# Kernel optimization log

Measured on AMD Instinct MI355X. Metric: run time of the kernel, lower is better.

## Reference

```python
import jax, jax.numpy as jnp
import numpy as np

DIM = 1024
HEAD_DIM = 64
NUM_HEADS = DIM // HEAD_DIM
SCALE = HEAD_DIM ** -0.5


def setup_inputs() -> dict:
    key = jax.random.key(0)
    ks = jax.random.split(key, 12)
    b, n = 4, 2048
    std = DIM ** -0.5
    inp = {
        'words': jax.random.normal(ks[0], (b, n, DIM), jnp.float32),
        'position': jax.random.normal(ks[1], (b, n, DIM), jnp.float32),
        'conscious': jax.random.normal(ks[2], (b, n, DIM), jnp.float32),
        # projection weights stored as [in, out] (torch Linear W^T)
        'w_wq': jax.random.normal(ks[3], (DIM, DIM), jnp.float32) * std,
        'w_wk': jax.random.normal(ks[4], (DIM, DIM), jnp.float32) * std,
        'w_wv': jax.random.normal(ks[5], (DIM, DIM), jnp.float32) * std,
        'w_pq': jax.random.normal(ks[6], (DIM, DIM), jnp.float32) * std,
        'w_pk': jax.random.normal(ks[7], (DIM, DIM), jnp.float32) * std,
        'w_cq': jax.random.normal(ks[8], (DIM, DIM), jnp.float32) * std,
        'w_ck': jax.random.normal(ks[9], (DIM, DIM), jnp.float32) * std,
        'w_out': jax.random.normal(ks[10], (DIM, DIM), jnp.float32) * std,
        'b_out': jax.random.normal(ks[11], (DIM,), jnp.float32) * 0.01,
    }
    return inp


def _heads(x):
    b, n, _ = x.shape
    return x.reshape(b, n, NUM_HEADS, HEAD_DIM).transpose(0, 2, 1, 3)  # b h n d


def reference(words, position, conscious, w_wq, w_wk, w_wv, w_pq, w_pk, w_cq, w_ck, w_out, b_out):
    # fused multi-source q/k: sum of three projections per source
    q = _heads(words @ w_wq + position @ w_pq + conscious @ w_cq)
    k = _heads(words @ w_wk + position @ w_pk + conscious @ w_ck)
    v = _heads(words @ w_wv)
    sim = jnp.einsum('bhid,bhjd->bhij', q, k) * SCALE
    attn = jax.nn.softmax(sim, axis=-1)
    out = jnp.einsum('bhij,bhjd->bhid', attn, v)
    b, h, n, d = out.shape
    out = out.transpose(0, 2, 1, 3).reshape(b, n, h * d)
    return out @ w_out + b_out
```

## Files before the change

### kernel.cpp

```cpp
#include <hip/hip_runtime.h>
#include <hip/hip_bf16.h>

typedef __bf16 bf16_t;
typedef __attribute__((ext_vector_type(8))) __bf16 bf16x8;
typedef __attribute__((ext_vector_type(4))) float f32x4;
typedef __attribute__((ext_vector_type(16))) float f32x16;

__device__ __forceinline__ void gld_lds16(const void* g, void* l) {
  __builtin_amdgcn_global_load_lds((const __attribute__((address_space(1))) void*)g,
                                   (__attribute__((address_space(3))) void*)l, 16, 0, 0);
}

__global__ __launch_bounds__(256) void cast_concat(
    const float* __restrict__ w, const float* __restrict__ p,
    const float* __restrict__ c, bf16_t* __restrict__ X)
{
  unsigned idx = blockIdx.x * 256u + threadIdx.x;
  unsigned src = idx >> 21;
  unsigned rem = idx & ((1u << 21) - 1);
  unsigned row = rem >> 8;
  unsigned k4  = (rem & 255u) * 4u;
  const float* s = (src == 0) ? w : (src == 1) ? p : c;
  f32x4 v = *(const f32x4*)(s + (size_t)row * 1024 + k4);
  ushort4 u;
  u.x = __builtin_bit_cast(unsigned short, (bf16_t)v[0]);
  u.y = __builtin_bit_cast(unsigned short, (bf16_t)v[1]);
  u.z = __builtin_bit_cast(unsigned short, (bf16_t)v[2]);
  u.w = __builtin_bit_cast(unsigned short, (bf16_t)v[3]);
  *(ushort4*)(X + (size_t)row * 3072 + src * 1024 + k4) = u;
}

__global__ __launch_bounds__(256) void transpose_all(
    const float* __restrict__ w_wq, const float* __restrict__ w_pq,
    const float* __restrict__ w_cq, const float* __restrict__ w_wk,
    const float* __restrict__ w_pk, const float* __restrict__ w_ck,
    const float* __restrict__ w_wv, const float* __restrict__ w_out,
    bf16_t* __restrict__ Wqkt, bf16_t* __restrict__ Wvt, bf16_t* __restrict__ Wot)
{
  __shared__ float t[32][33];
  const int z = blockIdx.z;
  const float* src; bf16_t* dst; int dstride, koff, roff;
  switch (z) {
    case 0: src = w_wq;  dst = Wqkt; dstride = 3072; koff = 0;    roff = 0;    break;
    case 1: src = w_pq;  dst = Wqkt; dstride = 3072; koff = 1024; roff = 0;    break;
    case 2: src = w_cq;  dst = Wqkt; dstride = 3072; koff = 2048; roff = 0;    break;
    case 3: src = w_wk;  dst = Wqkt; dstride = 3072; koff = 0;    roff = 1024; break;
    case 4: src = w_pk;  dst = Wqkt; dstride = 3072; koff = 1024; roff = 1024; break;
    case 5: src = w_ck;  dst = Wqkt; dstride = 3072; koff = 2048; roff = 1024; break;
    case 6: src = w_wv;  dst = Wvt;  dstride = 1024; koff = 0;    roff = 0;    break;
    default: src = w_out; dst = Wot; dstride = 1024; koff = 0;    roff = 0;    break;
  }
  int bx = blockIdx.x, by = blockIdx.y;
  int x = bx * 32 + threadIdx.x;
  int y0 = by * 32;
  for (int i = threadIdx.y; i < 32; i += 8)
    t[i][threadIdx.x] = src[(size_t)(y0 + i) * 1024 + x];
  __syncthreads();
  int n0 = bx * 32;
  for (int i = threadIdx.y; i < 32; i += 8)
    dst[(size_t)(n0 + i + roff) * dstride + koff + y0 + threadIdx.x] =
        (bf16_t)t[threadIdx.x][i];
}

__global__ __launch_bounds__(512, 2) void gemm256_qk(
    const bf16_t* __restrict__ A, int lda,
    const bf16_t* __restrict__ Bt, int K,
    bf16_t* __restrict__ Qo, bf16_t* __restrict__ Ko, float scale, int nbx)
{
  __shared__ bf16_t As[2][256 * 64];
  __shared__ bf16_t Bs[2][256 * 64];

  const int tid = threadIdx.x;
  const int wave = tid >> 6, lane = tid & 63;
  const int wm = wave >> 2, wn = wave & 3;
  const int lrow = lane & 15, lch = lane >> 4;

  const int nwg = gridDim.x, cpx = nwg >> 3;
  const int id  = blockIdx.x;
  const int swz = (id & 7) * cpx + (id >> 3);
  const int mb = swz / nbx, nb = swz % nbx;
  const int m0 = mb * 256, n0 = nb * 256;

  const int srow = tid >> 3, spp = tid & 7;

  auto STAGE = [&](int buf, int k0) {
#pragma unroll
    for (int i = 0; i < 4; ++i) {
      int r = i * 64 + srow;
      int gsw = (spp ^ (r & 7)) * 8;
      gld_lds16(A + (size_t)(m0 + r) * lda + k0 + gsw, &As[buf][r * 64 + spp * 8]);
    }
#pragma unroll
    for (int i = 0; i < 4; ++i) {
      int r = i * 64 + srow;
      int gsw = (spp ^ (r & 7)) * 8;
      gld_lds16(Bt + (size_t)(n0 + r) * K + k0 + gsw, &Bs[buf][r * 64 + spp * 8]);
    }
  };

  const int NT = K >> 6;
  STAGE(0, 0);
  STAGE(1, 64);

  f32x4 acc[8][4] = {};

  for (int kt = 0; kt < NT; ++kt) {
    const int cur = kt & 1;
    if (kt < NT - 1) {
      asm volatile("s_waitcnt vmcnt(8)" ::: "memory");
    } else {
      asm volatile("s_waitcnt vmcnt(0)" ::: "memory");
    }
    asm volatile("s_barrier" ::: "memory");

#pragma unroll
    for (int ks = 0; ks < 2; ++ks) {
      bf16x8 af[8], bfr[4];
#pragma unroll
      for (int m = 0; m < 8; ++m) {
        int r = wm * 128 + m * 16 + lrow;
        af[m] = *(const bf16x8*)&As[cur][r * 64 + (((ks * 4 + lch) ^ (r & 7)) * 8)];
      }
#pragma unroll
      for (int n = 0; n < 4; ++n) {
        int r = wn * 64 + n * 16 + lrow;
        bfr[n] = *(const bf16x8*)&Bs[cur][r * 64 + (((ks * 4 + lch) ^ (r & 7)) * 8)];
      }
      __builtin_amdgcn_s_setprio(1);
#pragma unroll
      for (int m = 0; m < 8; ++m)
#pragma unroll
        for (int n = 0; n < 4; ++n)
          acc[m][n] = __builtin_amdgcn_mfma_f32_16x16x32_bf16(af[m], bfr[n], acc[m][n], 0, 0, 0);
      __builtin_amdgcn_s_setprio(0);
    }

    asm volatile("s_waitcnt lgkmcnt(0)" ::: "memory");
    asm volatile("s_barrier" ::: "memory");
    if (kt + 2 < NT) STAGE(cur, (kt + 2) * 64);
  }

  const int g = lane >> 4, cl = lane & 15;
#pragma unroll
  for (int m = 0; m < 8; ++m) {
    int m_base = m0 + wm * 128 + m * 16 + g * 4;
    int bb = m_base >> 11, nn = m_base & 2047;
#pragma unroll
    for (int n = 0; n < 4; ++n) {
      int col = n0 + wn * 64 + n * 16 + cl;
      bf16_t* dst = (col < 1024) ? Qo : Ko;
      int cc2 = col & 1023;
      float sc = (col < 1024) ? scale : 1.0f;
      int h = cc2 >> 6, d = cc2 & 63;
      size_t base = ((size_t)(bb * 16 + h) * 2048 + nn) * 64 + d;
#pragma unroll
      for (int r = 0; r < 4; ++r)
        dst[base + (size_t)r * 64] = (bf16_t)(acc[m][n][r] * sc);
    }
  }
}

template<int EPI>
__global__ __launch_bounds__(256, 2) void gemm_bt(
    const bf16_t* __restrict__ A, int lda,
    const bf16_t* __restrict__ Bt, int K,
    void* __restrict__ Cout, const float* __restrict__ bias, float scale)
{
  __shared__ bf16_t As[128 * 32];
  __shared__ bf16_t Bs[128 * 32];
  const int tid  = threadIdx.x;
  const int wave = tid >> 6, lane = tid & 63;
  const int m0 = blockIdx.y * 128, n0 = blockIdx.x * 128;
  const int wr = (wave >> 1) * 64, wc = (wave & 1) * 64;
  const int lrow = lane & 15, lch = lane >> 4;

  f32x4 acc[4][4] = {};

  for (int k0 = 0; k0 < K; k0 += 32) {
    __syncthreads();
#pragma unroll
    for (int t = 0; t < 2; ++t) {
      int cc = t * 256 + tid;
      int row = cc >> 2, pp = cc & 3;
      int kswz = (pp ^ (row & 3)) * 8;
      gld_lds16(A  + (size_t)(m0 + row) * lda + k0 + kswz, &As[cc * 8]);
      gld_lds16(Bt + (size_t)(n0 + row) * K   + k0 + kswz, &Bs[cc * 8]);
    }
    __syncthreads();
    bf16x8 a[4], b[4];
#pragma unroll
    for (int i = 0; i < 4; ++i) {
      int r = wr + i * 16 + lrow;
      a[i] = *(const bf16x8*)&As[r * 32 + ((lch ^ (r & 3)) * 8)];
    }
#pragma unroll
    for (int i = 0; i < 4; ++i) {
      int r = wc + i * 16 + lrow;
      b[i] = *(const bf16x8*)&Bs[r * 32 + ((lch ^ (r & 3)) * 8)];
    }
#pragma unroll
    for (int i = 0; i < 4; ++i)
#pragma unroll
      for (int j = 0; j < 4; ++j)
        acc[i][j] = __builtin_amdgcn_mfma_f32_16x16x32_bf16(a[i], b[j], acc[i][j], 0, 0, 0);
  }

  const int g = lane >> 4, cl = lane & 15;
  if (EPI == 1) {
    bf16_t* Vo = (bf16_t*)Cout;
#pragma unroll
    for (int i = 0; i < 4; ++i) {
      int m_base = m0 + wr + i * 16 + g * 4;
      int bb = m_base >> 11, nn = m_base & 2047;
#pragma unroll
      for (int j = 0; j < 4; ++j) {
        int col = n0 + wc + j * 16 + cl;
        int h = col >> 6, d = col & 63;
        ushort4 u;
        u.x = __builtin_bit_cast(unsigned short, (bf16_t)acc[i][j][0]);
        u.y = __builtin_bit_cast(unsigned short, (bf16_t)acc[i][j][1]);
        u.z = __builtin_bit_cast(unsigned short, (bf16_t)acc[i][j][2]);
        u.w = __builtin_bit_cast(unsigned short, (bf16_t)acc[i][j][3]);
        *(ushort4*)(Vo + ((size_t)(bb * 16 + h) * 64 + d) * 2048 + nn) = u;
      }
    }
  } else {
    float* Co = (float*)Cout;
#pragma unroll
    for (int i = 0; i < 4; ++i) {
      int m_base = m0 + wr + i * 16 + g * 4;
#pragma unroll
      for (int j = 0; j < 4; ++j) {
        int col = n0 + wc + j * 16 + cl;
        float bv = bias[col];
#pragma unroll
        for (int r = 0; r < 4; ++r)
          Co[(size_t)(m_base + r) * 1024 + col] = acc[i][j][r] + bv;
      }
    }
  }
}

__global__ __launch_bounds__(512, 2) void attn_kernel(
    const bf16_t* __restrict__ Q, const bf16_t* __restrict__ Kb,
    const bf16_t* __restrict__ Vt, bf16_t* __restrict__ O)
{
  __shared__ bf16_t Ks[2][64 * 64];
  __shared__ bf16_t Vs[2][64 * 64];

  const int fid = blockIdx.x;
  const int swz = (fid & 7) * 64 + (fid >> 3);
  const int bh = swz >> 3, qt = swz & 7;
  const int bb = bh >> 4, h = bh & 15;

  const int tid = threadIdx.x, wave = tid >> 6, lane = tid & 63;
  const int lq = lane & 31;
  const int lh = lane >> 5;

  const bf16_t* Qb    = Q  + ((size_t)bh * 2048 + qt * 256) * 64;
  const bf16_t* Kbase = Kb + (size_t)bh * 2048 * 64;
  const bf16_t* Vbase = Vt + (size_t)bh * 64 * 2048;

  auto STAGE = [&](int buf, int kv0) {
    int row = tid >> 3, pp = tid & 7;
    int sgr = (pp ^ (row & 7)) * 8;
    gld_lds16(Kbase + (size_t)(kv0 + row) * 64 + sgr, &Ks[buf][tid * 8]);
    gld_lds16(Vbase + (size_t)row * 2048 + kv0 + sgr, &Vs[buf][tid * 8]);
  };

  STAGE(0, 0);

  bf16x8 qf[4];
#pragma unroll
  for (int kf = 0; kf < 4; ++kf)
    qf[kf] = *(const bf16x8*)(Qb + (size_t)(wave * 32 + lq) * 64 + kf * 16 + lh * 8);

  f32x16 acc[2] = {};
  float m_run = -1.0e30f, l_run = 0.f;

  for (int t = 0; t < 32; ++t) {
    const int buf = t & 1;
    if (t < 31) {
      STAGE(buf ^ 1, (t + 1) * 64);
      asm volatile("s_waitcnt vmcnt(2)" ::: "memory");
    } else {
      asm volatile("s_waitcnt vmcnt(0)" ::: "memory");
    }
    __builtin_amdgcn_s_barrier();
    asm volatile("" ::: "memory");

    f32x16 st[2] = {};
#pragma unroll
    for (int nb = 0; nb < 2; ++nb) {
      int r = nb * 32 + lq;
#pragma unroll
      for (int kf = 0; kf < 4; ++kf) {
        bf16x8 ka = *(const bf16x8*)&Ks[buf][r * 64 + (((kf * 2 + lh) ^ (r & 7)) * 8)];
        st[nb] = __builtin_amdgcn_mfma_f32_32x32x16_bf16(ka, qf[kf], st[nb], 0, 0, 0);
      }
    }

    float tmax = st[0][0];
#pragma unroll
    for (int nb = 0; nb < 2; ++nb)
#pragma unroll
      for (int rg = 0; rg < 16; ++rg)
        tmax = fmaxf(tmax, st[nb][rg]);
    tmax = fmaxf(tmax, __shfl_xor(tmax, 32));

    if (!__all(tmax <= m_run + 8.0f)) {
      float mnew = fmaxf(m_run, tmax);
      float corr = __builtin_amdgcn_exp2f(m_run - mnew);
      m_run = mnew;
      l_run *= corr;
#pragma unroll
      for (int db = 0; db < 2; ++db)
#pragma unroll
        for (int rg = 0; rg < 16; ++rg)
          acc[db][rg] *= corr;
    }

    float sm = 0.f;
#pragma unroll
    for (int nb = 0; nb < 2; ++nb)
#pragma unroll
      for (int rg = 0; rg < 16; ++rg) {
        float p = __builtin_amdgcn_exp2f(st[nb][rg] - m_run);
        st[nb][rg] = p;
        sm += p;
      }
    sm += __shfl_xor(sm, 32);
    l_run += sm;

#pragma unroll
    for (int ks = 0; ks < 4; ++ks) {
      const int nb = ks >> 1;
      const int R = (ks & 1) * 8;
      unsigned x0, x1, y0, y1;
      asm("v_cvt_pk_bf16_f32 %0, %1, %2" : "=v"(x0) : "v"(st[nb][R + 0]), "v"(st[nb][R + 1]));
      asm("v_cvt_pk_bf16_f32 %0, %1, %2" : "=v"(x1) : "v"(st[nb][R + 2]), "v"(st[nb][R + 3]));
      asm("v_cvt_pk_bf16_f32 %0, %1, %2" : "=v"(y0) : "v"(st[nb][R + 4]), "v"(st[nb][R + 5]));
      asm("v_cvt_pk_bf16_f32 %0, %1, %2" : "=v"(y1) : "v"(st[nb][R + 6]), "v"(st[nb][R + 7]));
      asm volatile("v_permlane32_swap_b32 %0, %1" : "+v"(x0), "+v"(y0));
      asm volatile("v_permlane32_swap_b32 %0, %1" : "+v"(x1), "+v"(y1));
      int4 pw;
      pw.x = (int)x0; pw.y = (int)x1; pw.z = (int)y0; pw.w = (int)y1;
      bf16x8 pb = __builtin_bit_cast(bf16x8, pw);
#pragma unroll
      for (int db = 0; db < 2; ++db) {
        int r = db * 32 + lq;
        bf16x8 va = *(const bf16x8*)&Vs[buf][r * 64 + (((ks * 2 + lh) ^ (r & 7)) * 8)];
        acc[db] = __builtin_amdgcn_mfma_f32_32x32x16_bf16(va, pb, acc[db], 0, 0, 0);
      }
    }

    asm volatile("s_waitcnt lgkmcnt(0)" ::: "memory");
    __builtin_amdgcn_s_barrier();
    asm volatile("" ::: "memory");
  }

  float inv = 1.0f / l_run;
  int nn = qt * 256 + wave * 32 + lq;
  size_t obase = ((size_t)bb * 2048 + nn) * 1024 + h * 64;
#pragma unroll
  for (int db = 0; db < 2; ++db)
#pragma unroll
    for (int rr = 0; rr < 4; ++rr) {
      ushort4 u;
      u.x = __builtin_bit_cast(unsigned short, (bf16_t)(acc[db][rr * 4 + 0] * inv));
      u.y = __builtin_bit_cast(unsigned short, (bf16_t)(acc[db][rr * 4 + 1] * inv));
      u.z = __builtin_bit_cast(unsigned short, (bf16_t)(acc[db][rr * 4 + 2] * inv));
      u.w = __builtin_bit_cast(unsigned short, (bf16_t)(acc[db][rr * 4 + 3] * inv));
      *(ushort4*)(O + obase + db * 32 + rr * 8 + lh * 4) = u;
    }
}

extern "C" void kernel_launch(void* const* d_in, const int* in_sizes, int n_in,
                              void* d_out, int out_size, void* d_ws, size_t ws_size,
                              hipStream_t stream) {
  const float* words     = (const float*)d_in[0];
  const float* position  = (const float*)d_in[1];
  const float* conscious = (const float*)d_in[2];
  const float* w_wq  = (const float*)d_in[3];
  const float* w_wk  = (const float*)d_in[4];
  const float* w_wv  = (const float*)d_in[5];
  const float* w_pq  = (const float*)d_in[6];
  const float* w_pk  = (const float*)d_in[7];
  const float* w_cq  = (const float*)d_in[8];
  const float* w_ck  = (const float*)d_in[9];
  const float* w_out = (const float*)d_in[10];
  const float* b_out = (const float*)d_in[11];

  char* ws = (char*)d_ws;
  bf16_t* Xcat = (bf16_t*)(ws);
  bf16_t* Wqkt = (bf16_t*)(ws + 50331648);
  bf16_t* Wvt  = (bf16_t*)(ws + 62914560);
  bf16_t* Wot  = (bf16_t*)(ws + 65011712);
  bf16_t* Qb   = (bf16_t*)(ws + 67108864);
  bf16_t* Kbf  = (bf16_t*)(ws + 83886080);
  bf16_t* Vtb  = (bf16_t*)(ws + 100663296);
  bf16_t* Ob   = (bf16_t*)(ws + 117440512);

  cast_concat<<<24576, 256, 0, stream>>>(words, position, conscious, Xcat);

  transpose_all<<<dim3(32, 32, 8), dim3(32, 8), 0, stream>>>(
      w_wq, w_pq, w_cq, w_wk, w_pk, w_ck, w_wv, w_out, Wqkt, Wvt, Wot);

  gemm256_qk<<<256, 512, 0, stream>>>(Xcat, 3072, Wqkt, 3072, Qb, Kbf,
                                      0.125f * 1.44269504f, 8);
  gemm_bt<1><<<dim3(8, 64), 256, 0, stream>>>(Xcat, 3072, Wvt, 1024, Vtb, nullptr, 1.0f);

  attn_kernel<<<512, 512, 0, stream>>>(Qb, Kbf, Vtb, Ob);

  gemm_bt<2><<<dim3(8, 64), 256, 0, stream>>>(Ob, 1024, Wot, 1024, (float*)d_out,
                                              b_out, 1.0f);
}
```

Measured before the change: 296.8 us.

## Replace V and output GEMMs with double-buffered 128x256 tile kernel

Swaps the simple 128x128, single-buffered, BK=32 GEMM used for the V projection and the output projection for a 512-thread 128x256-tile kernel. The new kernel uses BK=64, double-buffered LDS with async global-to-LDS loads, explicit vmcnt waits and barriers, MFMA priority hints, and an XCD-aware block swizzle. The aim is to overlap memory loads with MFMA work, halve the number of barriers per K, and get more reuse per tile. The trade-off is higher LDS use (96KB per block), which limits occupancy, and a grid of only 256 blocks.

```diff
diff --git a/kernel.cpp b/kernel.cpp
--- a/kernel.cpp
+++ b/kernel.cpp
@@ -161,81 +161,115 @@
 }
 
 template<int EPI>
-__global__ __launch_bounds__(256, 2) void gemm_bt(
+__global__ __launch_bounds__(512, 2) void gemm128x256(
     const bf16_t* __restrict__ A, int lda,
     const bf16_t* __restrict__ Bt, int K,
-    void* __restrict__ Cout, const float* __restrict__ bias, float scale)
+    void* __restrict__ Cout, const float* __restrict__ bias)
 {
-  __shared__ bf16_t As[128 * 32];
-  __shared__ bf16_t Bs[128 * 32];
-  const int tid  = threadIdx.x;
+  __shared__ bf16_t As[2][128 * 64];
+  __shared__ bf16_t Bs[2][256 * 64];
+
+  const int tid = threadIdx.x;
   const int wave = tid >> 6, lane = tid & 63;
-  const int m0 = blockIdx.y * 128, n0 = blockIdx.x * 128;
-  const int wr = (wave >> 1) * 64, wc = (wave & 1) * 64;
+  const int wm = wave >> 2, wn = wave & 3;
   const int lrow = lane & 15, lch = lane >> 4;
 
+  const int nwg = gridDim.x, cpx = nwg >> 3;
+  const int id  = blockIdx.x;
+  const int swz = (id & 7) * cpx + (id >> 3);
+  const int mb = swz >> 2, nb = swz & 3;
+  const int m0 = mb * 128, n0 = nb * 256;
+
+  const int srow = tid >> 3, spp = tid & 7;
+
+  auto STAGE = [&](int buf, int k0) {
+#pragma unroll
+    for (int i = 0; i < 2; ++i) {
+      int r = i * 64 + srow;
+      int gsw = (spp ^ (r & 7)) * 8;
+      gld_lds16(A + (size_t)(m0 + r) * lda + k0 + gsw, &As[buf][r * 64 + spp * 8]);
+    }
+#pragma unroll
+    for (int i = 0; i < 4; ++i) {
+      int r = i * 64 + srow;
+      int gsw = (spp ^ (r & 7)) * 8;
+      gld_lds16(Bt + (size_t)(n0 + r) * K + k0 + gsw, &Bs[buf][r * 64 + spp * 8]);
+    }
+  };
+
+  const int NT = K >> 6;
+  STAGE(0, 0);
+  STAGE(1, 64);
+
   f32x4 acc[4][4] = {};
 
-  for (int k0 = 0; k0 < K; k0 += 32) {
-    __syncthreads();
-#pragma unroll
-    for (int t = 0; t < 2; ++t) {
-      int cc = t * 256 + tid;
-      int row = cc >> 2, pp = cc & 3;
-      int kswz = (pp ^ (row & 3)) * 8;
-      gld_lds16(A  + (size_t)(m0 + row) * lda + k0 + kswz, &As[cc * 8]);
-      gld_lds16(Bt + (size_t)(n0 + row) * K   + k0 + kswz, &Bs[cc * 8]);
-    }
-    __syncthreads();
-    bf16x8 a[4], b[4];
-#pragma unroll
-    for (int i = 0; i < 4; ++i) {
-      int r = wr + i * 16 + lrow;
-      a[i] = *(const bf16x8*)&As[r * 32 + ((lch ^ (r & 3)) * 8)];
-    }
-#pragma unroll
-    for (int i = 0; i < 4; ++i) {
-      int r = wc + i * 16 + lrow;
-      b[i] = *(const bf16x8*)&Bs[r * 32 + ((lch ^ (r & 3)) * 8)];
-    }
-#pragma unroll
-    for (int i = 0; i < 4; ++i)
-#pragma unroll
-      for (int j = 0; j < 4; ++j)
-        acc[i][j] = __builtin_amdgcn_mfma_f32_16x16x32_bf16(a[i], b[j], acc[i][j], 0, 0, 0);
+  for (int kt = 0; kt < NT; ++kt) {
+    const int cur = kt & 1;
+    if (kt < NT - 1) {
+      asm volatile("s_waitcnt vmcnt(6)" ::: "memory");
+    } else {
+      asm volatile("s_waitcnt vmcnt(0)" ::: "memory");
+    }
+    asm volatile("s_barrier" ::: "memory");
+
+#pragma unroll
+    for (int ks = 0; ks < 2; ++ks) {
+      bf16x8 af[4], bfr[4];
+#pragma unroll
+      for (int m = 0; m < 4; ++m) {
+        int r = wm * 64 + m * 16 + lrow;
+        af[m] = *(const bf16x8*)&As[cur][r * 64 + (((ks * 4 + lch) ^ (r & 7)) * 8)];
+      }
+#pragma unroll
+      for (int n = 0; n < 4; ++n) {
+        int r = wn * 64 + n * 16 + lrow;
+        bfr[n] = *(const bf16x8*)&Bs[cur][r * 64 + (((ks * 4 + lch) ^ (r & 7)) * 8)];
+      }
+      __builtin_amdgcn_s_setprio(1);
+#pragma unroll
+      for (int m = 0; m < 4; ++m)
+#pragma unroll
+        for (int n = 0; n < 4; ++n)
+          acc[m][n] = __builtin_amdgcn_mfma_f32_16x16x32_bf16(af[m], bfr[n], acc[m][n], 0, 0, 0);
+      __builtin_amdgcn_s_setprio(0);
+    }
+
+    asm volatile("s_waitcnt lgkmcnt(0)" ::: "memory");
+    asm volatile("s_barrier" ::: "memory");
+    if (kt + 2 < NT) STAGE(cur, (kt + 2) * 64);
   }
 
   const int g = lane >> 4, cl = lane & 15;
   if (EPI == 1) {
     bf16_t* Vo = (bf16_t*)Cout;
 #pragma unroll
-    for (int i = 0; i < 4; ++i) {
-      int m_base = m0 + wr + i * 16 + g * 4;
+    for (int m = 0; m < 4; ++m) {
+      int m_base = m0 + wm * 64 + m * 16 + g * 4;
       int bb = m_base >> 11, nn = m_base & 2047;
 #pragma unroll
-      for (int j = 0; j < 4; ++j) {
-        int col = n0 + wc + j * 16 + cl;
+      for (int n = 0; n < 4; ++n) {
+        int col = n0 + wn * 64 + n * 16 + cl;
         int h = col >> 6, d = col & 63;
         ushort4 u;
-        u.x = __builtin_bit_cast(unsigned short, (bf16_t)acc[i][j][0]);
-        u.y = __builtin_bit_cast(unsigned short, (bf16_t)acc[i][j][1]);
-        u.z = __builtin_bit_cast(unsigned short, (bf16_t)acc[i][j][2]);
-        u.w = __builtin_bit_cast(unsigned short, (bf16_t)acc[i][j][3]);
+        u.x = __builtin_bit_cast(unsigned short, (bf16_t)acc[m][n][0]);
+        u.y = __builtin_bit_cast(unsigned short, (bf16_t)acc[m][n][1]);
+        u.z = __builtin_bit_cast(unsigned short, (bf16_t)acc[m][n][2]);
+        u.w = __builtin_bit_cast(unsigned short, (bf16_t)acc[m][n][3]);
         *(ushort4*)(Vo + ((size_t)(bb * 16 + h) * 64 + d) * 2048 + nn) = u;
       }
     }
   } else {
     float* Co = (float*)Cout;
 #pragma unroll
-    for (int i = 0; i < 4; ++i) {
-      int m_base = m0 + wr + i * 16 + g * 4;
-#pragma unroll
-      for (int j = 0; j < 4; ++j) {
-        int col = n0 + wc + j * 16 + cl;
+    for (int m = 0; m < 4; ++m) {
+      int m_base = m0 + wm * 64 + m * 16 + g * 4;
+#pragma unroll
+      for (int n = 0; n < 4; ++n) {
+        int col = n0 + wn * 64 + n * 16 + cl;
         float bv = bias[col];
 #pragma unroll
         for (int r = 0; r < 4; ++r)
-          Co[(size_t)(m_base + r) * 1024 + col] = acc[i][j][r] + bv;
+          Co[(size_t)(m_base + r) * 1024 + col] = acc[m][n][r] + bv;
       }
     }
   }
@@ -408,10 +442,9 @@
 
   gemm256_qk<<<256, 512, 0, stream>>>(Xcat, 3072, Wqkt, 3072, Qb, Kbf,
                                       0.125f * 1.44269504f, 8);
-  gemm_bt<1><<<dim3(8, 64), 256, 0, stream>>>(Xcat, 3072, Wvt, 1024, Vtb, nullptr, 1.0f);
+  gemm128x256<1><<<256, 512, 0, stream>>>(Xcat, 3072, Wvt, 1024, Vtb, nullptr);
 
   attn_kernel<<<512, 512, 0, stream>>>(Qb, Kbf, Vtb, Ob);
 
-  gemm_bt<2><<<dim3(8, 64), 256, 0, stream>>>(Ob, 1024, Wot, 1024, (float*)d_out,
-                                              b_out, 1.0f);
-}
+  gemm128x256<2><<<256, 512, 0, stream>>>(Ob, 1024, Wot, 1024, (float*)d_out, b_out);
+}
```

New measurement: 288.9 us. -2.7%, faster.
